# Performance work log

Hardware: AMD Instinct MI355X
Metric: run time of the kernel (lower is better)

## Reference

```python
import jax, jax.numpy as jnp
import numpy as np

N2, N1, N0 = 16000, 4000, 1000   # leaf / mid / target node counts
DEG = 32                          # sampled neighbors per target
IN_DIM, OUT_DIM, H = 256, 64, 4
NEG = -9e15
ALPHA = 0.2                       # LeakyReLU slope


def setup_inputs() -> dict:
    key = jax.random.key(0)
    ks = jax.random.split(key, 10)
    s = 0.05  # xavier-ish scale
    x = jax.random.normal(ks[0], (N2, IN_DIM), jnp.float32)
    W0 = jax.random.normal(ks[1], (H, IN_DIM, OUT_DIM), jnp.float32) * s
    a0 = jax.random.normal(ks[2], (H, 2 * OUT_DIM), jnp.float32) * s
    W1 = jax.random.normal(ks[3], (H, OUT_DIM * H, OUT_DIM), jnp.float32) * s
    a1 = jax.random.normal(ks[4], (H, 2 * OUT_DIM), jnp.float32) * s
    lin_W = jax.random.normal(ks[5], (OUT_DIM * H, OUT_DIM * H), jnp.float32) * s
    lin_b = jax.random.normal(ks[6], (OUT_DIM * H,), jnp.float32) * s
    # level-1 edges: n1 targets, each with DEG sampled leaf neighbors + self-loop
    adj1_tgt = jnp.concatenate([jnp.repeat(jnp.arange(N1), DEG), jnp.arange(N1)]).astype(jnp.int32)
    adj1_nbr = jnp.concatenate([jax.random.randint(ks[7], (N1 * DEG,), 0, N2),
                                jnp.arange(N1)]).astype(jnp.int32)
    # level-0 edges: n0 targets, each with DEG sampled mid neighbors + self-loop
    adj0_tgt = jnp.concatenate([jnp.repeat(jnp.arange(N0), DEG), jnp.arange(N0)]).astype(jnp.int32)
    adj0_nbr = jnp.concatenate([jax.random.randint(ks[8], (N0 * DEG,), 0, N1),
                                jnp.arange(N0)]).astype(jnp.int32)
    return {"x": x, "W0": W0, "a0": a0, "W1": W1, "a1": a1,
            "lin_W": lin_W, "lin_b": lin_b,
            "adj1_tgt": adj1_tgt, "adj1_nbr": adj1_nbr,
            "adj0_tgt": adj0_tgt, "adj0_nbr": adj0_nbr,
            "n0": N0, "n1": N1}


def _att_layer(x, W, a, tgt, nbr, T):
    # x: [N, D], W: [H, D, O], a: [H, 2O]; multi-head GAT layer (eval mode, no dropout)
    h = jnp.einsum('nd,hdo->hno', x, W)                      # [H, N, O]
    O = h.shape[-1]
    e = jax.nn.leaky_relu(
        jnp.einsum('heo,ho->he', h[:, tgt], a[:, :O]) +
        jnp.einsum('heo,ho->he', h[:, nbr], a[:, O:]), ALPHA)  # [H, E]
    N = h.shape[1]
    att = jnp.full((h.shape[0], T, N), NEG, x.dtype).at[:, tgt, nbr].set(e)
    att = jax.nn.softmax(att, axis=-1)                        # dense edge-softmax
    hp = jax.nn.elu(jnp.einsum('htn,hno->hto', att, h))       # [H, T, O]
    return jnp.transpose(hp, (1, 0, 2)).reshape(T, -1)        # cat heads -> [T, H*O]


def reference(x, W0, a0, W1, a1, lin_W, lin_b,
              adj1_tgt, adj1_nbr, adj0_tgt, adj0_nbr, n0, n1):
    x1 = _att_layer(x, W0, a0, adj1_tgt, adj1_nbr, n1)   # [n1, H*O]
    x2 = _att_layer(x1, W1, a1, adj0_tgt, adj0_nbr, n0)  # [n0, H*O]
    return jnp.tanh(x2 @ lin_W.T + lin_b)                # Linear + Tanh
```

## Files before the change

kernel.cpp:

```cpp
#include <hip/hip_runtime.h>
#include <math.h>

#define N2C 16000
#define N1C 4000
#define N0C 1000
#define DEG 32
#define CH 256
#define NHEAD 4
#define ODIM 64
#define ALPHA 0.2f
#define LDP 264
#define EPAD 36

typedef __attribute__((ext_vector_type(8))) short bf16x8;
typedef __attribute__((ext_vector_type(4))) float f32x4;

__device__ __forceinline__ ushort f2bf(float f) {
    unsigned u = __float_as_uint(f);
    unsigned r = (u + 0x7fffu + ((u >> 16) & 1u)) >> 16;
    return (ushort)r;
}
__device__ __forceinline__ float bf2f(ushort h) {
    return __uint_as_float(((unsigned)h) << 16);
}

__global__ __launch_bounds__(256) void repack_kernel(
    const float* __restrict__ W0, const float* __restrict__ W1,
    const float* __restrict__ linW,
    ushort* __restrict__ Wth, ushort* __restrict__ Wtl)
{
    int g = blockIdx.x * 256 + threadIdx.x;
    int mat = g >> 16;
    int idx = g & 65535;
    int c = idx >> 8, k = idx & 255;
    float v;
    if (mat == 0)      v = W0[(c >> 6) * (256 * 64) + k * 64 + (c & 63)];
    else if (mat == 1) v = W1[(c >> 6) * (256 * 64) + k * 64 + (c & 63)];
    else               v = linW[c * 256 + k];
    ushort h = f2bf(v);
    Wth[g] = h;
    Wtl[g] = f2bf(v - bf2f(h));
}

template<int RT, int EPI, int AF32, int SC>
__global__ __launch_bounds__(256) void gemm_mfma(
    const float* __restrict__ Af,
    const ushort* __restrict__ Ah, const ushort* __restrict__ Al,
    const ushort* __restrict__ Bh, const ushort* __restrict__ Bl,
    const float* __restrict__ bias, const float* __restrict__ avec,
    float* __restrict__ out, float* __restrict__ s_t, float* __restrict__ s_n, int M)
{
    __shared__ ushort sah[AF32 ? RT * 16 * LDP : 1];
    __shared__ ushort sal[AF32 ? RT * 16 * LDP : 1];

    const int wave = threadIdx.x >> 6;
    const int lane = threadIdx.x & 63;
    const int quad = lane >> 4, l16 = lane & 15;
    const int row0 = blockIdx.x * (RT * 16);
    const int col0 = wave * 64;

    if (AF32) {
        for (int idx = threadIdx.x; idx < RT * 16 * 64; idx += 256) {
            int row = idx >> 6, c4 = idx & 63;
            int gr = row0 + row; if (gr >= M) gr = M - 1;
            float4 f = ((const float4*)Af)[gr * 64 + c4];
            ushort4 h, l;
            h.x = f2bf(f.x); l.x = f2bf(f.x - bf2f(h.x));
            h.y = f2bf(f.y); l.y = f2bf(f.y - bf2f(h.y));
            h.z = f2bf(f.z); l.z = f2bf(f.z - bf2f(h.z));
            h.w = f2bf(f.w); l.w = f2bf(f.w - bf2f(h.w));
            *(ushort4*)(&sah[row * LDP + c4 * 4]) = h;
            *(ushort4*)(&sal[row * LDP + c4 * 4]) = l;
        }
        __syncthreads();
    }

    f32x4 acc[RT][4];
#pragma unroll
    for (int r = 0; r < RT; ++r)
#pragma unroll
        for (int c = 0; c < 4; ++c) acc[r][c] = (f32x4){0.f, 0.f, 0.f, 0.f};

    int arow[RT];
#pragma unroll
    for (int r = 0; r < RT; ++r) {
        int rr = row0 + r * 16 + l16;
        arow[r] = (rr < M) ? rr : (M - 1);
    }
    const int kbase = quad * 8;

    for (int k0 = 0; k0 < 256; k0 += 32) {
        bf16x8 a_h[RT], a_l[RT], b_h[4], b_l[4];
#pragma unroll
        for (int r = 0; r < RT; ++r) {
            if (AF32) {
                int loff = (r * 16 + l16) * LDP + k0 + kbase;
                a_h[r] = *(const bf16x8*)(&sah[loff]);
                a_l[r] = *(const bf16x8*)(&sal[loff]);
            } else {
                int off = arow[r] * 256 + k0 + kbase;
                a_h[r] = *(const bf16x8*)(Ah + off);
                a_l[r] = *(const bf16x8*)(Al + off);
            }
        }
#pragma unroll
        for (int c = 0; c < 4; ++c) {
            int off = (col0 + c * 16 + l16) * 256 + k0 + kbase;
            b_h[c] = *(const bf16x8*)(Bh + off);
            b_l[c] = *(const bf16x8*)(Bl + off);
        }
#pragma unroll
        for (int r = 0; r < RT; ++r)
#pragma unroll
            for (int c = 0; c < 4; ++c) {
                acc[r][c] = __builtin_amdgcn_mfma_f32_16x16x32_bf16(a_h[r], b_h[c], acc[r][c], 0, 0, 0);
                acc[r][c] = __builtin_amdgcn_mfma_f32_16x16x32_bf16(a_h[r], b_l[c], acc[r][c], 0, 0, 0);
                acc[r][c] = __builtin_amdgcn_mfma_f32_16x16x32_bf16(a_l[r], b_h[c], acc[r][c], 0, 0, 0);
            }
    }

#pragma unroll
    for (int r = 0; r < RT; ++r)
#pragma unroll
        for (int c = 0; c < 4; ++c) {
            int col = col0 + c * 16 + l16;
#pragma unroll
            for (int reg = 0; reg < 4; ++reg) {
                int row = row0 + r * 16 + quad * 4 + reg;
                if (row < M) {
                    float v = acc[r][c][reg];
                    if (EPI == 1) v = tanhf(v + bias[col]);
                    out[row * 256 + col] = v;
                }
            }
        }

    if (SC) {
        float at[4], an[4];
#pragma unroll
        for (int c = 0; c < 4; ++c) {
            at[c] = avec[wave * 128 + c * 16 + l16];
            an[c] = avec[wave * 128 + 64 + c * 16 + l16];
        }
#pragma unroll
        for (int r = 0; r < RT; ++r) {
            float pt[4] = {0.f, 0.f, 0.f, 0.f}, pn[4] = {0.f, 0.f, 0.f, 0.f};
#pragma unroll
            for (int c = 0; c < 4; ++c)
#pragma unroll
                for (int reg = 0; reg < 4; ++reg) {
                    pt[reg] += acc[r][c][reg] * at[c];
                    pn[reg] += acc[r][c][reg] * an[c];
                }
#pragma unroll
            for (int reg = 0; reg < 4; ++reg)
#pragma unroll
                for (int m = 1; m < 16; m <<= 1) {
                    pt[reg] += __shfl_xor(pt[reg], m);
                    pn[reg] += __shfl_xor(pn[reg], m);
                }
            if (l16 == 0) {
#pragma unroll
                for (int reg = 0; reg < 4; ++reg) {
                    int row = row0 + r * 16 + quad * 4 + reg;
                    if (row < M) {
                        s_t[wave * M + row] = pt[reg];
                        s_n[wave * M + row] = pn[reg];
                    }
                }
            }
        }
    }
}

__global__ __launch_bounds__(256) void att_kernel(
    const float* __restrict__ hprev, const int* __restrict__ nbr_arr,
    const float* __restrict__ s_t, const float* __restrict__ s_n,
    ushort* __restrict__ outhi, ushort* __restrict__ outlo, int T, int Nsrc)
{
    __shared__ int nbr[EPAD];
    __shared__ float att_s[NHEAD][EPAD];
    __shared__ float4 red[4][64];
    const int tgt = blockIdx.x;
    const int t = threadIdx.x;
    const int lane = t & 63;
    if (t < DEG) nbr[t] = nbr_arr[tgt * DEG + t];
    else if (t == DEG) nbr[DEG] = nbr_arr[T * DEG + tgt];
    else if (t < EPAD) nbr[t] = 0;
    __syncthreads();

    {
        const int hd = t >> 6;
        int me = (lane <= DEG) ? nbr[lane] : 0;
        int k = (lane <= DEG) ? 1 : 0;
#pragma unroll
        for (int j = 0; j < DEG; ++j) {
            int v = __shfl(me, j);
            if (j < lane && v == me && lane <= DEG) k = 0;
        }
        float e = s_t[hd * Nsrc + tgt] + s_n[hd * Nsrc + me];
        e = (e >= 0.f) ? e : ALPHA * e;
        float em = k ? e : -1e30f;
        float m = em;
#pragma unroll
        for (int off = 1; off < 64; off <<= 1) m = fmaxf(m, __shfl_xor(m, off));
        float w = k ? __expf(e - m) : 0.f;
        float Z = w;
#pragma unroll
        for (int off = 1; off < 64; off <<= 1) Z += __shfl_xor(Z, off);
        if (lane < EPAD) att_s[hd][lane] = (lane <= DEG) ? (w / Z) : 0.f;
    }
    __syncthreads();

    const int cq = t & 63;
    const int rg = t >> 6;
    const int hd = cq >> 4;
    const float4* hp4 = (const float4*)hprev;
    float w[9];
    int rrow[9];
#pragma unroll
    for (int ii = 0; ii < 9; ++ii) {
        w[ii] = att_s[hd][rg * 9 + ii];
        rrow[ii] = nbr[rg * 9 + ii];
    }
    float4 acc = make_float4(0.f, 0.f, 0.f, 0.f);
#pragma unroll
    for (int ii = 0; ii < 9; ++ii) {
        float4 v = hp4[(size_t)rrow[ii] * 64 + cq];
        acc.x += w[ii] * v.x; acc.y += w[ii] * v.y;
        acc.z += w[ii] * v.z; acc.w += w[ii] * v.w;
    }
    red[rg][cq] = acc;
    __syncthreads();
    if (t < 64) {
        float4 s0 = red[0][t], s1 = red[1][t], s2 = red[2][t], s3 = red[3][t];
        float4 s;
        s.x = s0.x + s1.x + s2.x + s3.x;
        s.y = s0.y + s1.y + s2.y + s3.y;
        s.z = s0.z + s1.z + s2.z + s3.z;
        s.w = s0.w + s1.w + s2.w + s3.w;
        s.x = (s.x > 0.f) ? s.x : expm1f(s.x);
        s.y = (s.y > 0.f) ? s.y : expm1f(s.y);
        s.z = (s.z > 0.f) ? s.z : expm1f(s.z);
        s.w = (s.w > 0.f) ? s.w : expm1f(s.w);
        ushort4 h, l;
        h.x = f2bf(s.x); l.x = f2bf(s.x - bf2f(h.x));
        h.y = f2bf(s.y); l.y = f2bf(s.y - bf2f(h.y));
        h.z = f2bf(s.z); l.z = f2bf(s.z - bf2f(h.z));
        h.w = f2bf(s.w); l.w = f2bf(s.w - bf2f(h.w));
        ((ushort4*)outhi)[tgt * 64 + t] = h;
        ((ushort4*)outlo)[tgt * 64 + t] = l;
    }
}

extern "C" void kernel_launch(void* const* d_in, const int* in_sizes, int n_in,
                              void* d_out, int out_size, void* d_ws, size_t ws_size,
                              hipStream_t stream)
{
    const float* x    = (const float*)d_in[0];
    const float* W0   = (const float*)d_in[1];
    const float* a0   = (const float*)d_in[2];
    const float* W1   = (const float*)d_in[3];
    const float* a1   = (const float*)d_in[4];
    const float* linW = (const float*)d_in[5];
    const float* linb = (const float*)d_in[6];
    const int* adj1_nbr = (const int*)d_in[8];
    const int* adj0_nbr = (const int*)d_in[10];

    char* base = (char*)d_ws;
    ushort* Wth = (ushort*)base;
    ushort* Wtl = Wth + 3 * 65536;
    float*  st  = (float*)(base + 786432);
    float*  sn  = st + 65536;
    float*  h0  = (float*)(base + 1310720);
    ushort* xhi = (ushort*)(base + 1310720 + 16384000);
    ushort* xlo = xhi + 4096000;

    repack_kernel<<<768, 256, 0, stream>>>(W0, W1, linW, Wth, Wtl);

    gemm_mfma<2, 0, 1, 1><<<N2C / 32, 256, 0, stream>>>(
        x, nullptr, nullptr, Wth, Wtl, nullptr, a0, h0, st, sn, N2C);
    att_kernel<<<N1C, 256, 0, stream>>>(h0, adj1_nbr, st, sn, xhi, xlo, N1C, N2C);

    gemm_mfma<1, 0, 0, 1><<<N1C / 16, 256, 0, stream>>>(
        nullptr, xhi, xlo, Wth + 65536, Wtl + 65536, nullptr, a1, h0, st, sn, N1C);
    att_kernel<<<N0C, 256, 0, stream>>>(h0, adj0_nbr, st, sn, xhi, xlo, N0C, N1C);

    gemm_mfma<1, 1, 0, 0><<<(N0C + 15) / 16, 256, 0, stream>>>(
        nullptr, xhi, xlo, Wth + 131072, Wtl + 131072, linb, nullptr,
        (float*)d_out, nullptr, nullptr, N0C);
}
```

Before: 167.4 us.

## Fuse all stages into one persistent kernel with software grid barriers

Replaces the six separate launches (repack, two GEMM/attention pairs, final linear) with one persistent kernel of 512 blocks. The blocks walk each stage's tiles in a strided loop and separate stages with atomic-counter grid barriers. This removes per-launch overhead and the idle gaps between dependent kernels. In exchange it relies on all 512 blocks being co-resident, adds barrier spin cost, caps parallelism in stages that have few tiles, and allocates the GEMM's shared memory in every stage.

```diff
diff --git a/kernel.cpp b/kernel.cpp
--- a/kernel.cpp
+++ b/kernel.cpp
@@ -11,6 +11,7 @@
 #define ALPHA 0.2f
 #define LDP 264
 #define EPAD 36
+#define GRIDN 512
 
 typedef __attribute__((ext_vector_type(8))) short bf16x8;
 typedef __attribute__((ext_vector_type(4))) float f32x4;
@@ -24,39 +25,40 @@
     return __uint_as_float(((unsigned)h) << 16);
 }
 
-__global__ __launch_bounds__(256) void repack_kernel(
-    const float* __restrict__ W0, const float* __restrict__ W1,
-    const float* __restrict__ linW,
-    ushort* __restrict__ Wth, ushort* __restrict__ Wtl)
-{
-    int g = blockIdx.x * 256 + threadIdx.x;
-    int mat = g >> 16;
-    int idx = g & 65535;
-    int c = idx >> 8, k = idx & 255;
-    float v;
-    if (mat == 0)      v = W0[(c >> 6) * (256 * 64) + k * 64 + (c & 63)];
-    else if (mat == 1) v = W1[(c >> 6) * (256 * 64) + k * 64 + (c & 63)];
-    else               v = linW[c * 256 + k];
-    ushort h = f2bf(v);
-    Wth[g] = h;
-    Wtl[g] = f2bf(v - bf2f(h));
+__device__ __forceinline__ void grid_barrier(unsigned* bar, int idx) {
+    __syncthreads();
+    if (threadIdx.x == 0) {
+        __threadfence();
+        __hip_atomic_fetch_add(bar + idx, 1u, __ATOMIC_RELEASE, __HIP_MEMORY_SCOPE_AGENT);
+        int spins = 0;
+        while (__hip_atomic_load(bar + idx, __ATOMIC_ACQUIRE, __HIP_MEMORY_SCOPE_AGENT)
+               < (unsigned)GRIDN) {
+            __builtin_amdgcn_s_sleep(2);
+            if (++spins > 500000) break;
+        }
+        __threadfence();
+    }
+    __syncthreads();
+}
+
+__global__ __launch_bounds__(64) void init_kernel(unsigned* bar) {
+    if (threadIdx.x < 8) bar[threadIdx.x] = 0;
 }
 
 template<int RT, int EPI, int AF32, int SC>
-__global__ __launch_bounds__(256) void gemm_mfma(
+__device__ __forceinline__ void gemm_tile(
+    int tileIdx, int M,
     const float* __restrict__ Af,
     const ushort* __restrict__ Ah, const ushort* __restrict__ Al,
     const ushort* __restrict__ Bh, const ushort* __restrict__ Bl,
     const float* __restrict__ bias, const float* __restrict__ avec,
-    float* __restrict__ out, float* __restrict__ s_t, float* __restrict__ s_n, int M)
+    float* __restrict__ out, float* __restrict__ s_t, float* __restrict__ s_n,
+    ushort* sah, ushort* sal)
 {
-    __shared__ ushort sah[AF32 ? RT * 16 * LDP : 1];
-    __shared__ ushort sal[AF32 ? RT * 16 * LDP : 1];
-
     const int wave = threadIdx.x >> 6;
     const int lane = threadIdx.x & 63;
     const int quad = lane >> 4, l16 = lane & 15;
-    const int row0 = blockIdx.x * (RT * 16);
+    const int row0 = tileIdx * (RT * 16);
     const int col0 = wave * 64;
 
     if (AF32) {
@@ -173,15 +175,13 @@
     }
 }
 
-__global__ __launch_bounds__(256) void att_kernel(
+__device__ __forceinline__ void att_tile(
+    int tgt,
     const float* __restrict__ hprev, const int* __restrict__ nbr_arr,
     const float* __restrict__ s_t, const float* __restrict__ s_n,
-    ushort* __restrict__ outhi, ushort* __restrict__ outlo, int T, int Nsrc)
+    ushort* __restrict__ outhi, ushort* __restrict__ outlo, int T, int Nsrc,
+    int* nbr, float (*att_s)[EPAD], float4 (*red)[64])
 {
-    __shared__ int nbr[EPAD];
-    __shared__ float att_s[NHEAD][EPAD];
-    __shared__ float4 red[4][64];
-    const int tgt = blockIdx.x;
     const int t = threadIdx.x;
     const int lane = t & 63;
     if (t < DEG) nbr[t] = nbr_arr[tgt * DEG + t];
@@ -251,6 +251,69 @@
         ((ushort4*)outhi)[tgt * 64 + t] = h;
         ((ushort4*)outlo)[tgt * 64 + t] = l;
     }
+    __syncthreads();
+}
+
+__global__ __launch_bounds__(256, 2) void mega_kernel(
+    const float* __restrict__ x,
+    const float* __restrict__ W0, const float* __restrict__ a0,
+    const float* __restrict__ W1, const float* __restrict__ a1,
+    const float* __restrict__ linW, const float* __restrict__ linb,
+    const int* __restrict__ adj1_nbr, const int* __restrict__ adj0_nbr,
+    char* __restrict__ ws, float* __restrict__ dout)
+{
+    __shared__ ushort sah[2 * 16 * LDP];
+    __shared__ ushort sal[2 * 16 * LDP];
+    __shared__ int nbr[EPAD];
+    __shared__ float att_s[NHEAD][EPAD];
+    __shared__ float4 red[4][64];
+
+    const int bid = blockIdx.x;
+
+    ushort* Wth = (ushort*)ws;
+    ushort* Wtl = Wth + 3 * 65536;
+    float*  st  = (float*)(ws + 786432);
+    float*  sn  = (float*)(ws + 1048576);
+    unsigned* bar = (unsigned*)(ws + 1304576);
+    float*  h0  = (float*)(ws + 1310720);
+    ushort* xhi = (ushort*)(ws + 1310720 + 16384000);
+    ushort* xlo = xhi + 4096000;
+
+    for (int g = bid * 256 + threadIdx.x; g < 3 * 65536; g += GRIDN * 256) {
+        int mat = g >> 16;
+        int idx = g & 65535;
+        int c = idx >> 8, k = idx & 255;
+        float v;
+        if (mat == 0)      v = W0[(c >> 6) * (256 * 64) + k * 64 + (c & 63)];
+        else if (mat == 1) v = W1[(c >> 6) * (256 * 64) + k * 64 + (c & 63)];
+        else               v = linW[c * 256 + k];
+        ushort h = f2bf(v);
+        Wth[g] = h;
+        Wtl[g] = f2bf(v - bf2f(h));
+    }
+    grid_barrier(bar, 0);
+
+    for (int tile = bid; tile < N2C / 32; tile += GRIDN)
+        gemm_tile<2, 0, 1, 1>(tile, N2C, x, nullptr, nullptr, Wth, Wtl,
+                              nullptr, a0, h0, st, sn, sah, sal);
+    grid_barrier(bar, 1);
+
+    for (int tgt = bid; tgt < N1C; tgt += GRIDN)
+        att_tile(tgt, h0, adj1_nbr, st, sn, xhi, xlo, N1C, N2C, nbr, att_s, red);
+    grid_barrier(bar, 2);
+
+    for (int tile = bid; tile < N1C / 16; tile += GRIDN)
+        gemm_tile<1, 0, 0, 1>(tile, N1C, nullptr, xhi, xlo, Wth + 65536, Wtl + 65536,
+                              nullptr, a1, h0, st, sn, sah, sal);
+    grid_barrier(bar, 3);
+
+    for (int tgt = bid; tgt < N0C; tgt += GRIDN)
+        att_tile(tgt, h0, adj0_nbr, st, sn, xhi, xlo, N0C, N1C, nbr, att_s, red);
+    grid_barrier(bar, 4);
+
+    for (int tile = bid; tile < (N0C + 15) / 16; tile += GRIDN)
+        gemm_tile<1, 1, 0, 0>(tile, N0C, nullptr, xhi, xlo, Wth + 131072, Wtl + 131072,
+                              linb, nullptr, dout, nullptr, nullptr, sah, sal);
 }
 
 extern "C" void kernel_launch(void* const* d_in, const int* in_sizes, int n_in,
@@ -266,27 +329,9 @@
     const float* linb = (const float*)d_in[6];
     const int* adj1_nbr = (const int*)d_in[8];
     const int* adj0_nbr = (const int*)d_in[10];
-
-    char* base = (char*)d_ws;
-    ushort* Wth = (ushort*)base;
-    ushort* Wtl = Wth + 3 * 65536;
-    float*  st  = (float*)(base + 786432);
-    float*  sn  = st + 65536;
-    float*  h0  = (float*)(base + 1310720);
-    ushort* xhi = (ushort*)(base + 1310720 + 16384000);
-    ushort* xlo = xhi + 4096000;
-
-    repack_kernel<<<768, 256, 0, stream>>>(W0, W1, linW, Wth, Wtl);
-
-    gemm_mfma<2, 0, 1, 1><<<N2C / 32, 256, 0, stream>>>(
-        x, nullptr, nullptr, Wth, Wtl, nullptr, a0, h0, st, sn, N2C);
-    att_kernel<<<N1C, 256, 0, stream>>>(h0, adj1_nbr, st, sn, xhi, xlo, N1C, N2C);
-
-    gemm_mfma<1, 0, 0, 1><<<N1C / 16, 256, 0, stream>>>(
-        nullptr, xhi, xlo, Wth + 65536, Wtl + 65536, nullptr, a1, h0, st, sn, N1C);
-    att_kernel<<<N0C, 256, 0, stream>>>(h0, adj0_nbr, st, sn, xhi, xlo, N0C, N1C);
-
-    gemm_mfma<1, 1, 0, 0><<<(N0C + 15) / 16, 256, 0, stream>>>(
-        nullptr, xhi, xlo, Wth + 131072, Wtl + 131072, linb, nullptr,
-        (float*)d_out, nullptr, nullptr, N0C);
-}
+    char* ws = (char*)d_ws;
+
+    init_kernel<<<1, 64, 0, stream>>>((unsigned*)(ws + 1304576));
+    mega_kernel<<<GRIDN, 256, 0, stream>>>(
+        x, W0, a0, W1, a1, linW, linb, adj1_nbr, adj0_nbr, ws, (float*)d_out);
+}
```

New measurement: 587.4 us. +250.9%, slower.
